# Performance work log

Hardware: AMD Instinct MI355X
Metric: run time of the kernel (lower is better)

## Reference

```python
import jax, jax.numpy as jnp
import numpy as np

B, S, D = 2, 2048, 1024
H = 16
HD = D // H  # 64
SCALE = HD ** 0.5


def setup_inputs() -> dict:
    key = jax.random.key(0)
    ks = jax.random.split(key, 7)
    return {
        "query": jax.random.normal(ks[0], (B, S, D), dtype=jnp.float32),
        "key": jax.random.normal(ks[1], (B, S, D), dtype=jnp.float32),
        "value": jax.random.normal(ks[2], (B, S, D), dtype=jnp.float32),
        "W_qkv_w": jax.random.normal(ks[3], (3 * D, 3 * D), dtype=jnp.float32) * (1.0 / np.sqrt(3 * D)),
        "W_qkv_b": jax.random.normal(ks[4], (3 * D,), dtype=jnp.float32) * 0.02,
        "W_o_w": jax.random.normal(ks[5], (D, D), dtype=jnp.float32) * (1.0 / np.sqrt(D)),
        "W_o_b": jax.random.normal(ks[6], (D,), dtype=jnp.float32) * 0.02,
    }


def _split_heads(x):
    # [B,S,D] -> [B,H,S,HD]
    return x.reshape(B, S, H, HD).transpose(0, 2, 1, 3)


def reference(query, key, value, W_qkv_w, W_qkv_b, W_o_w, W_o_b):
    # fused QKV projection: concat then Linear(3D, 3D)  (torch: x @ W.T + b)
    qkv = jnp.concatenate([query, key, value], axis=-1)
    qkv = qkv @ W_qkv_w.T + W_qkv_b
    q, k, v = jnp.split(qkv, 3, axis=-1)
    q, k, v = _split_heads(q), _split_heads(k), _split_heads(v)
    # naive attention: materializes [B,H,S,S]
    scores = jnp.einsum('bhqd,bhkd->bhqk', q, k) / SCALE
    probs = jax.nn.softmax(scores, axis=-1)
    attn = jnp.einsum('bhqk,bhkd->bhqd', probs, v)
    # combine heads: [B,H,S,HD] -> [B,S,D]
    attn = attn.transpose(0, 2, 1, 3).reshape(B, S, D)
    return attn @ W_o_w.T + W_o_b
```

## Files before the change

### kernel.cpp

```cpp
#include <hip/hip_runtime.h>
#include <cmath>

#define BS   2
#define SEQ  2048
#define DM   1024
#define NH   16
#define HD   64
#define D3   3072
#define MROWS 4096
#define KVBLK 64
#define QBLK  128
#define NTILES (SEQ / KVBLK)

#define CSC 0.18033688011112042f

typedef _Float16 f16;
typedef __attribute__((ext_vector_type(4))) _Float16 half4;
typedef __attribute__((ext_vector_type(8))) _Float16 half8;
typedef __attribute__((ext_vector_type(4))) float f32x4;
typedef unsigned int u32;
typedef __attribute__((ext_vector_type(2))) u32 u32x2;
typedef __attribute__((ext_vector_type(4))) u32 u32x4;

__device__ __forceinline__ void async_cp16(const void* g, void* s) {
    __builtin_amdgcn_global_load_lds(
        (const __attribute__((address_space(1))) u32*)g,
        (__attribute__((address_space(3))) u32*)s, 16, 0, 0);
}

__global__ __launch_bounds__(256) void conv_concat_kernel(
    const float* __restrict__ q, const float* __restrict__ k,
    const float* __restrict__ v, f16* __restrict__ out)
{
    const int seg = blockIdx.x;
    const int row = blockIdx.y;
    const int c   = threadIdx.x * 4;
    const float* src = (seg == 0 ? q : (seg == 1 ? k : v)) + (size_t)row * DM + c;
    float4 x = *(const float4*)src;
    half4 h = {(f16)x.x, (f16)x.y, (f16)x.z, (f16)x.w};
    *(half4*)&out[(size_t)row * D3 + seg * DM + c] = h;
}

__global__ __launch_bounds__(256) void conv_plain_kernel(
    const float* __restrict__ src, f16* __restrict__ dst, int n4)
{
    int i = blockIdx.x * 256 + threadIdx.x;
    const int stride = gridDim.x * 256;
    for (; i < n4; i += stride) {
        float4 x = *(const float4*)&src[(size_t)i * 4];
        half4 h = {(f16)x.x, (f16)x.y, (f16)x.z, (f16)x.w};
        *(half4*)&dst[(size_t)i * 4] = h;
    }
}

template<int KDIM, int NDIM, bool F16OUT>
__global__ __launch_bounds__(256) void gemm_f16_kernel(
    const f16* __restrict__ A, const f16* __restrict__ W,
    const float* __restrict__ bias, void* __restrict__ Cout)
{
    __shared__ f16 As[128 * 32];
    __shared__ f16 Ws[128 * 32];

    const int tid  = threadIdx.x;
    const int lane = tid & 63;
    const int wave = tid >> 6;
    const int l15  = lane & 15;
    const int lg   = lane >> 4;
    const int wm   = wave >> 1;
    const int wn   = wave & 1;

    const int cpx = gridDim.x >> 3;
    const int lid = (blockIdx.x & 7) * cpx + (blockIdx.x >> 3);
    const int NT  = NDIM / 128;
    const int tM0 = (lid / NT) * 128;
    const int tN0 = (lid % NT) * 128;

    const int srow = lane >> 2;
    const int sch  = lane & 3;
    const int ssc  = sch ^ ((srow >> 1) & 3);

    const f16* gA0 = A + (size_t)(tM0 + wave * 32      + srow) * KDIM + ssc * 8;
    const f16* gA1 = A + (size_t)(tM0 + wave * 32 + 16 + srow) * KDIM + ssc * 8;
    const f16* gW0 = W + (size_t)(tN0 + wave * 32      + srow) * KDIM + ssc * 8;
    const f16* gW1 = W + (size_t)(tN0 + wave * 32 + 16 + srow) * KDIM + ssc * 8;
    f16* lA0 = &As[(wave * 32)      * 32];
    f16* lA1 = &As[(wave * 32 + 16) * 32];
    f16* lW0 = &Ws[(wave * 32)      * 32];
    f16* lW1 = &Ws[(wave * 32 + 16) * 32];

    f32x4 acc[4][4];
#pragma unroll
    for (int i = 0; i < 4; ++i)
#pragma unroll
        for (int j = 0; j < 4; ++j) acc[i][j] = (f32x4){0.f, 0.f, 0.f, 0.f};

    const int fsw = (lg ^ ((l15 >> 1) & 3)) * 8;
    int aoff[4], woff[4];
#pragma unroll
    for (int mi = 0; mi < 4; ++mi) aoff[mi] = (wm * 64 + mi * 16 + l15) * 32 + fsw;
#pragma unroll
    for (int ni = 0; ni < 4; ++ni) woff[ni] = (wn * 64 + ni * 16 + l15) * 32 + fsw;

    for (int k0 = 0; k0 < KDIM; k0 += 32) {
        __syncthreads();
        async_cp16(gA0 + k0, lA0);
        async_cp16(gA1 + k0, lA1);
        async_cp16(gW0 + k0, lW0);
        async_cp16(gW1 + k0, lW1);
        __syncthreads();

        half8 af[4], wf[4];
#pragma unroll
        for (int mi = 0; mi < 4; ++mi) af[mi] = *(half8*)&As[aoff[mi]];
#pragma unroll
        for (int ni = 0; ni < 4; ++ni) wf[ni] = *(half8*)&Ws[woff[ni]];
#pragma unroll
        for (int mi = 0; mi < 4; ++mi)
#pragma unroll
            for (int ni = 0; ni < 4; ++ni)
                acc[mi][ni] = __builtin_amdgcn_mfma_f32_16x16x32_f16(
                    af[mi], wf[ni], acc[mi][ni], 0, 0, 0);
    }

    float bv[4];
#pragma unroll
    for (int ni = 0; ni < 4; ++ni) bv[ni] = bias[tN0 + wn * 64 + ni * 16 + l15];

#pragma unroll
    for (int mi = 0; mi < 4; ++mi)
#pragma unroll
        for (int ni = 0; ni < 4; ++ni)
#pragma unroll
            for (int r = 0; r < 4; ++r) {
                const int m   = tM0 + wm * 64 + mi * 16 + lg * 4 + r;
                const int col = tN0 + wn * 64 + ni * 16 + l15;
                const float val = acc[mi][ni][r] + bv[ni];
                if constexpr (F16OUT)
                    ((f16*)Cout)[(size_t)m * NDIM + col] = (f16)val;
                else
                    ((float*)Cout)[(size_t)m * NDIM + col] = val;
            }
}


#define V_STORE(VtN, va, vb) do {                                             \
    u32x4 aw_ = __builtin_bit_cast(u32x4, va);                                \
    u32x4 bw_ = __builtin_bit_cast(u32x4, vb);                                \
    _Pragma("unroll")                                                         \
    for (int wd_ = 0; wd_ < 4; ++wd_) {                                       \
        u32 lo_ = __builtin_amdgcn_perm(bw_[wd_], aw_[wd_], 0x05040100u);     \
        u32 hi_ = __builtin_amdgcn_perm(bw_[wd_], aw_[wd_], 0x07060302u);     \
        const int dl_ = vd0 + 2 * wd_;                                        \
        const int dh_ = dl_ + 1;                                              \
        *(u32*)&VtN[dl_ * KVBLK + (((vp >> 2) ^ (dl_ & 7) ^ (dl_ >> 3)) * 8)  \
                    + 2 * (vp & 3)] = lo_;                                    \
        *(u32*)&VtN[dh_ * KVBLK + (((vp >> 2) ^ (dh_ & 7) ^ (dh_ >> 3)) * 8)  \
                    + 2 * (vp & 3)] = hi_;                                    \
    }                                                                         \
} while (0)

#define ATTN_STEP(KhC, VtC, KhN, VtN, TT, PF) do {                            \
    half8 va_ = {}, vb_ = {};                                                 \
    if (PF) {                                                                 \
        const size_t nro_ = (size_t)((TT) + 1) * KVBLK;                       \
        async_cp16(kxsrc + (nro_ + wave * 16 +     krow_l) * D3,              \
                   &KhN[(wave * 16) * HD]);                                   \
        async_cp16(kxsrc + (nro_ + wave * 16 + 8 + krow_l) * D3,              \
                   &KhN[(wave * 16 + 8) * HD]);                               \
        va_ = *(const half8*)(vsrc0 + nro_ * D3);                             \
        vb_ = *(const half8*)(vsrc0 + nro_ * D3 + D3);                        \
    }                                                                         \
    f32x4 sc[2][4];                                                           \
    _Pragma("unroll")                                                         \
    for (int rt = 0; rt < 2; ++rt)                                            \
        _Pragma("unroll")                                                     \
        for (int ct = 0; ct < 4; ++ct) sc[rt][ct] = (f32x4){0.f,0.f,0.f,0.f}; \
    __builtin_amdgcn_s_setprio(1);                                            \
    _Pragma("unroll")                                                         \
    for (int ct = 0; ct < 4; ++ct) {                                          \
        const int krow = ct * 16 + l15;                                       \
        _Pragma("unroll")                                                     \
        for (int ks = 0; ks < 2; ++ks) {                                      \
            half8 kf = *(half8*)&KhC[krow * HD +                              \
                                     (((ks * 4 + lg) ^ (krow & 7)) * 8)];     \
            _Pragma("unroll")                                                 \
            for (int rt = 0; rt < 2; ++rt)                                    \
                sc[rt][ct] = __builtin_amdgcn_mfma_f32_16x16x32_f16(          \
                    kf, qf[rt][ks], sc[rt][ct], 0, 0, 0);                     \
        }                                                                     \
    }                                                                         \
    __builtin_amdgcn_s_setprio(0);                                            \
    _Pragma("unroll")                                                         \
    for (int rt = 0; rt < 2; ++rt) {                                          \
        float mt = sc[rt][0][0];                                              \
        _Pragma("unroll")                                                     \
        for (int ct = 0; ct < 4; ++ct)                                        \
            _Pragma("unroll")                                                 \
            for (int r = 0; r < 4; ++r)                                       \
                if (ct || r) mt = fmaxf(mt, sc[rt][ct][r]);                   \
        mt = fmaxf(mt, __shfl_xor(mt, 16));                                   \
        mt = fmaxf(mt, __shfl_xor(mt, 32));                                   \
        const float mn = fmaxf(mrun[rt], mt * CSC);                           \
        const float alpha = exp2f(mrun[rt] - mn);                             \
        mrun[rt] = mn;                                                        \
        float pv_[4][4];                                                      \
        float ls = 0.f;                                                       \
        _Pragma("unroll")                                                     \
        for (int ct = 0; ct < 4; ++ct)                                        \
            _Pragma("unroll")                                                 \
            for (int r = 0; r < 4; ++r) {                                     \
                pv_[ct][r] = exp2f(fmaf(sc[rt][ct][r], CSC, -mn));            \
                ls += pv_[ct][r];                                             \
            }                                                                 \
        ls += __shfl_xor(ls, 16);                                             \
        ls += __shfl_xor(ls, 32);                                             \
        lrun[rt] = lrun[rt] * alpha + ls;                                     \
        _Pragma("unroll")                                                     \
        for (int dct = 0; dct < 4; ++dct)                                     \
            _Pragma("unroll")                                                 \
            for (int r = 0; r < 4; ++r) oacc[rt][dct][r] *= alpha;            \
        const int prow_ = pbase + (rt * 16 + l15) * KVBLK;                    \
        _Pragma("unroll")                                                     \
        for (int ct = 0; ct < 4; ++ct) {                                      \
            u32 w01 = __builtin_bit_cast(u32,                                 \
                __builtin_amdgcn_cvt_pkrtz(pv_[ct][0], pv_[ct][1]));          \
            u32 w23 = __builtin_bit_cast(u32,                                 \
                __builtin_amdgcn_cvt_pkrtz(pv_[ct][2], pv_[ct][3]));          \
            *(u32x2*)&Pl[prow_ + ((4 * ct + lg) ^ l15) * 4] =                 \
                (u32x2){w01, w23};                                            \
        }                                                                     \
    }                                                                         \
    __builtin_amdgcn_s_setprio(1);                                            \
    _Pragma("unroll")                                                         \
    for (int ks2 = 0; ks2 < 2; ++ks2) {                                       \
        half8 pa[2];                                                          \
        _Pragma("unroll")                                                     \
        for (int rt = 0; rt < 2; ++rt) {                                      \
            const int prow_ = pbase + (rt * 16 + l15) * KVBLK;                \
            half4 plA_ = *(half4*)&Pl[prow_ + ((8 * ks2 + 2 * lg)     ^ l15) * 4]; \
            half4 plB_ = *(half4*)&Pl[prow_ + ((8 * ks2 + 2 * lg + 1) ^ l15) * 4]; \
            pa[rt] = __builtin_shufflevector(plA_, plB_, 0,1,2,3,4,5,6,7);    \
        }                                                                     \
        _Pragma("unroll")                                                     \
        for (int dct = 0; dct < 4; ++dct) {                                   \
            const int d = dct * 16 + l15;                                     \
            half8 vf = *(half8*)&VtC[d * KVBLK +                              \
                        (((ks2 * 4 + lg) ^ (d & 7) ^ (d >> 3)) * 8)];         \
            _Pragma("unroll")                                                 \
            for (int rt = 0; rt < 2; ++rt)                                    \
                oacc[rt][dct] = __builtin_amdgcn_mfma_f32_16x16x32_f16(       \
                    vf, pa[rt], oacc[rt][dct], 0, 0, 0);                      \
        }                                                                     \
    }                                                                         \
    __builtin_amdgcn_s_setprio(0);                                            \
    if (PF) { V_STORE(VtN, va_, vb_); }                                       \
    __syncthreads();                                                          \
} while (0)

__global__ __launch_bounds__(256, 2) void attn_mfma_kernel(
    const f16* __restrict__ qkvh, f16* __restrict__ attnh)
{
    __shared__ f16 Kh0[KVBLK * HD];
    __shared__ f16 Kh1[KVBLK * HD];
    __shared__ f16 Vt0[HD * KVBLK];
    __shared__ f16 Vt1[HD * KVBLK];
    __shared__ f16 Pl[4 * 32 * KVBLK];

    const int tid  = threadIdx.x;
    const int lane = tid & 63;
    const int wave = tid >> 6;
    const int l15  = lane & 15;
    const int lg   = lane >> 4;

    const int nq  = SEQ / QBLK;
    const int cpx = gridDim.x >> 3;
    const int lid = (blockIdx.x & 7) * cpx + (blockIdx.x >> 3);
    const int b   = lid / (NH * nq);
    const int h   = (lid / nq) % NH;
    const int qc  = lid % nq;
    const int q0  = qc * QBLK + wave * 32;
    const size_t bS = (size_t)b * SEQ;

    const int krow_l = lane >> 3;
    const int kschk  = (lane & 7) ^ krow_l;
    const f16* kxsrc = qkvh + bS * D3 + DM + h * HD + kschk * 8;

    const int vp  = tid >> 3;
    const int vd0 = (tid & 7) * 8;
    const f16* vsrc0 = qkvh + (bS + 2 * vp) * D3 + 2 * DM + h * HD + vd0;

    half8 qf[2][2];
#pragma unroll
    for (int rt = 0; rt < 2; ++rt)
#pragma unroll
        for (int ks = 0; ks < 2; ++ks)
            qf[rt][ks] = *(const half8*)&qkvh[(bS + q0 + rt * 16 + l15) * D3 +
                                              h * HD + ks * 32 + lg * 8];

    f32x4 oacc[2][4];
#pragma unroll
    for (int rt = 0; rt < 2; ++rt)
#pragma unroll
        for (int dct = 0; dct < 4; ++dct) oacc[rt][dct] = (f32x4){0.f, 0.f, 0.f, 0.f};

    float mrun[2], lrun[2];
#pragma unroll
    for (int rt = 0; rt < 2; ++rt) { mrun[rt] = -INFINITY; lrun[rt] = 0.f; }

    const int pbase = wave * 32 * KVBLK;

    {
        async_cp16(kxsrc + (size_t)(wave * 16 +     krow_l) * D3, &Kh0[(wave * 16) * HD]);
        async_cp16(kxsrc + (size_t)(wave * 16 + 8 + krow_l) * D3, &Kh0[(wave * 16 + 8) * HD]);
        half8 va_ = *(const half8*)(vsrc0);
        half8 vb_ = *(const half8*)(vsrc0 + D3);
        V_STORE(Vt0, va_, vb_);
        __syncthreads();
    }

    for (int t = 0; t < NTILES; t += 2) {
        ATTN_STEP(Kh0, Vt0, Kh1, Vt1, t, true);
        ATTN_STEP(Kh1, Vt1, Kh0, Vt0, t + 1, (t + 1) < (NTILES - 1));
    }

#pragma unroll
    for (int rt = 0; rt < 2; ++rt) {
        const float inv = 1.f / lrun[rt];
        const int qq = q0 + rt * 16 + l15;
#pragma unroll
        for (int dct = 0; dct < 4; ++dct) {
            half4 o;
#pragma unroll
            for (int r = 0; r < 4; ++r) o[r] = (f16)(oacc[rt][dct][r] * inv);
            *(half4*)&attnh[(bS + qq) * DM + h * HD + dct * 16 + 4 * lg] = o;
        }
    }
}

extern "C" void kernel_launch(void* const* d_in, const int* in_sizes, int n_in,
                              void* d_out, int out_size, void* d_ws, size_t ws_size,
                              hipStream_t stream) {
    const float* q    = (const float*)d_in[0];
    const float* k    = (const float*)d_in[1];
    const float* v    = (const float*)d_in[2];
    const float* Wqkv = (const float*)d_in[3];
    const float* bqkv = (const float*)d_in[4];
    const float* Wo   = (const float*)d_in[5];
    const float* bo   = (const float*)d_in[6];
    float* out = (float*)d_out;

    char* ws = (char*)d_ws;
    f16* Ain    = (f16*)ws;
    f16* attn_h = (f16*)ws;
    f16* Wo_h   = (f16*)(ws + 16777216);
    f16* Wqkv_h = (f16*)(ws + 25165824);
    f16* qkv_h  = (f16*)(ws + 44040192);

    conv_concat_kernel<<<dim3(3, MROWS), 256, 0, stream>>>(q, k, v, Ain);
    conv_plain_kernel<<<2048, 256, 0, stream>>>(Wqkv, Wqkv_h, D3 * D3 / 4);

    gemm_f16_kernel<D3, D3, true><<<dim3((MROWS / 128) * (D3 / 128)), 256, 0, stream>>>(
        Ain, Wqkv_h, bqkv, qkv_h);

    attn_mfma_kernel<<<dim3(BS * NH * (SEQ / QBLK)), 256, 0, stream>>>(qkv_h, attn_h);

    conv_plain_kernel<<<512, 256, 0, stream>>>(Wo, Wo_h, DM * DM / 4);

    gemm_f16_kernel<DM, DM, false><<<dim3((MROWS / 128) * (DM / 128)), 256, 0, stream>>>(
        attn_h, Wo_h, bo, out);
}
```

Measured before the change: 215.7 us.

## Triple-buffer GEMM shared-memory tiles with async prefetch and vmcnt waits

Turns the f16 GEMM K-loop from one shared buffer with two barriers per step into a three-stage ring of shared-memory tiles. Async global-to-LDS copies for tiles k+1 and k+2 are issued while MFMAs run on tile k, and completion is tracked with `s_waitcnt vmcnt(4)` plus a single barrier per step. This is meant to hide global load latency behind matrix math. It triples the GEMM's LDS footprint, which may lower occupancy. At the tail no new stage is issued, so `vmcnt(4)` may not actually wait for the final tile, leaving a possible race.

```diff
diff --git a/kernel.cpp b/kernel.cpp
--- a/kernel.cpp
+++ b/kernel.cpp
@@ -53,13 +53,40 @@
     }
 }
 
+#define GSTAGE(B, K0) do {                                                    \
+    async_cp16(gA0 + (K0), &As[B][(wave * 32)      * 32]);                    \
+    async_cp16(gA1 + (K0), &As[B][(wave * 32 + 16) * 32]);                    \
+    async_cp16(gW0 + (K0), &Ws[B][(wave * 32)      * 32]);                    \
+    async_cp16(gW1 + (K0), &Ws[B][(wave * 32 + 16) * 32]);                    \
+} while (0)
+
+#define GCOMPUTE(B) do {                                                      \
+    half8 af[4], wf[4];                                                       \
+    _Pragma("unroll")                                                         \
+    for (int mi = 0; mi < 4; ++mi) af[mi] = *(half8*)&As[B][aoff[mi]];        \
+    _Pragma("unroll")                                                         \
+    for (int ni = 0; ni < 4; ++ni) wf[ni] = *(half8*)&Ws[B][woff[ni]];        \
+    _Pragma("unroll")                                                         \
+    for (int mi = 0; mi < 4; ++mi)                                            \
+        _Pragma("unroll")                                                     \
+        for (int ni = 0; ni < 4; ++ni)                                        \
+            acc[mi][ni] = __builtin_amdgcn_mfma_f32_16x16x32_f16(             \
+                af[mi], wf[ni], acc[mi][ni], 0, 0, 0);                        \
+} while (0)
+
+#define VWAIT_BAR() do {                                                      \
+    asm volatile("s_waitcnt vmcnt(4)" ::: "memory");                          \
+    __builtin_amdgcn_s_barrier();                                             \
+    __builtin_amdgcn_sched_barrier(0);                                        \
+} while (0)
+
 template<int KDIM, int NDIM, bool F16OUT>
 __global__ __launch_bounds__(256) void gemm_f16_kernel(
     const f16* __restrict__ A, const f16* __restrict__ W,
     const float* __restrict__ bias, void* __restrict__ Cout)
 {
-    __shared__ f16 As[128 * 32];
-    __shared__ f16 Ws[128 * 32];
+    __shared__ f16 As[3][128 * 32];
+    __shared__ f16 Ws[3][128 * 32];
 
     const int tid  = threadIdx.x;
     const int lane = tid & 63;
@@ -71,9 +98,9 @@
 
     const int cpx = gridDim.x >> 3;
     const int lid = (blockIdx.x & 7) * cpx + (blockIdx.x >> 3);
-    const int NT  = NDIM / 128;
-    const int tM0 = (lid / NT) * 128;
-    const int tN0 = (lid % NT) * 128;
+    const int NT2 = NDIM / 128;
+    const int tM0 = (lid / NT2) * 128;
+    const int tN0 = (lid % NT2) * 128;
 
     const int srow = lane >> 2;
     const int sch  = lane & 3;
@@ -83,10 +110,6 @@
     const f16* gA1 = A + (size_t)(tM0 + wave * 32 + 16 + srow) * KDIM + ssc * 8;
     const f16* gW0 = W + (size_t)(tN0 + wave * 32      + srow) * KDIM + ssc * 8;
     const f16* gW1 = W + (size_t)(tN0 + wave * 32 + 16 + srow) * KDIM + ssc * 8;
-    f16* lA0 = &As[(wave * 32)      * 32];
-    f16* lA1 = &As[(wave * 32 + 16) * 32];
-    f16* lW0 = &Ws[(wave * 32)      * 32];
-    f16* lW1 = &Ws[(wave * 32 + 16) * 32];
 
     f32x4 acc[4][4];
 #pragma unroll
@@ -101,25 +124,25 @@
 #pragma unroll
     for (int ni = 0; ni < 4; ++ni) woff[ni] = (wn * 64 + ni * 16 + l15) * 32 + fsw;
 
-    for (int k0 = 0; k0 < KDIM; k0 += 32) {
-        __syncthreads();
-        async_cp16(gA0 + k0, lA0);
-        async_cp16(gA1 + k0, lA1);
-        async_cp16(gW0 + k0, lW0);
-        async_cp16(gW1 + k0, lW1);
-        __syncthreads();
-
-        half8 af[4], wf[4];
-#pragma unroll
-        for (int mi = 0; mi < 4; ++mi) af[mi] = *(half8*)&As[aoff[mi]];
-#pragma unroll
-        for (int ni = 0; ni < 4; ++ni) wf[ni] = *(half8*)&Ws[woff[ni]];
-#pragma unroll
-        for (int mi = 0; mi < 4; ++mi)
-#pragma unroll
-            for (int ni = 0; ni < 4; ++ni)
-                acc[mi][ni] = __builtin_amdgcn_mfma_f32_16x16x32_f16(
-                    af[mi], wf[ni], acc[mi][ni], 0, 0, 0);
+    constexpr int NT = KDIM / 32;
+
+    GSTAGE(0, 0);
+    GSTAGE(1, 32);
+    VWAIT_BAR();
+
+    for (int t = 0; t < NT; t += 3) {
+        const int kb = t * 32;
+        if (t + 2 < NT) GSTAGE(2, kb + 64);
+        GCOMPUTE(0);
+        VWAIT_BAR();
+        if (t + 1 >= NT) break;
+        if (t + 3 < NT) GSTAGE(0, kb + 96);
+        GCOMPUTE(1);
+        VWAIT_BAR();
+        if (t + 2 >= NT) break;
+        if (t + 4 < NT) GSTAGE(1, kb + 128);
+        GCOMPUTE(2);
+        VWAIT_BAR();
     }
 
     float bv[4];
```

New measurement: 262.8 us. 21.8% more time.
